# Kernel tuning notes

Measured on AMD Instinct MI355X. Metric: run time of the kernel, lower is better.

Reference implementation:

```python
import jax, jax.numpy as jnp
import numpy as np

N, E, D, R = 50000, 600000, 128, 8


def rgcn_conv(x, src, dst, etype, W, root, bias):
    """PyG-style RGCNConv with mean aggregation per relation.
    x: [N, Din]; W: [R, Din, Dout]; root: [Din, Dout]; bias: [Dout]."""
    n = x.shape[0]
    r = W.shape[0]
    # Transform once per relation at node level (cheaper than per-edge matmul).
    xw = jnp.einsum('nd,rdo->rno', x, W)  # [R, N, Dout]
    # Per-(relation, target) edge counts for mean normalization.
    seg = etype * n + dst                  # combined segment id in [0, R*N)
    counts = jax.ops.segment_sum(jnp.ones(src.shape, dtype=x.dtype), seg,
                                 num_segments=r * n)
    norm = 1.0 / jnp.maximum(counts[seg], 1.0)   # [E]
    msg = xw[etype, src] * norm[:, None]          # gather per edge, [E, Dout]
    agg = jax.ops.segment_sum(msg, dst, num_segments=n)  # scatter-add, [N, Dout]
    return agg + x @ root + bias


def setup_inputs() -> dict:
    key = jax.random.key(0)
    ks = jax.random.split(key, 16)
    s = 1.0 / np.sqrt(D)
    inp = {
        'x': jax.random.normal(ks[0], (N, D), dtype=jnp.float32),
        'edge_index': jax.random.randint(ks[1], (2, E), 0, N, dtype=jnp.int32),
        'edge_type': jax.random.randint(ks[2], (E,), 0, R, dtype=jnp.int32),
        'W1': jax.random.normal(ks[3], (R, D, D), dtype=jnp.float32) * s,
        'root1': jax.random.normal(ks[4], (D, D), dtype=jnp.float32) * s,
        'b1': jnp.zeros((D,), dtype=jnp.float32),
        'W2': jax.random.normal(ks[5], (R, D, D), dtype=jnp.float32) * s,
        'root2': jax.random.normal(ks[6], (D, D), dtype=jnp.float32) * s,
        'b2': jnp.zeros((D,), dtype=jnp.float32),
        'W3': jax.random.normal(ks[7], (R, D, D), dtype=jnp.float32) * s,
        'root3': jax.random.normal(ks[8], (D, D), dtype=jnp.float32) * s,
        'b3': jnp.zeros((D,), dtype=jnp.float32),
        'res_w': jax.random.normal(ks[9], (D, D), dtype=jnp.float32) * s,
        'res_b': jnp.zeros((D,), dtype=jnp.float32),
    }
    return inp


def reference(x, edge_index, edge_type, W1, root1, b1, W2, root2, b2,
              W3, root3, b3, res_w, res_b):
    src, dst = edge_index[0], edge_index[1]
    res = x @ res_w + res_b
    h = jax.nn.relu(rgcn_conv(x, src, dst, edge_type, W1, root1, b1))
    h = res + jax.nn.relu(h)
    h = jax.nn.relu(rgcn_conv(h, src, dst, edge_type, W2, root2, b2))
    h = res + jax.nn.relu(h)
    h = jax.nn.relu(rgcn_conv(h, src, dst, edge_type, W3, root3, b3))
    h = res + jax.nn.relu(h)
    # Dropout(0.05) is identity in eval mode.
    return h
```

## Files before the change

kernel.cpp:

```cpp
#include <hip/hip_runtime.h>
#include <hip/hip_bf16.h>

#define NN 50000
#define EE 600000
#define RR 8
#define NSEG (NN*RR)
#define NB_SCAN ((NSEG + 1023)/1024)

typedef unsigned int u32;
typedef __attribute__((ext_vector_type(8))) short bf16x8;
typedef __attribute__((ext_vector_type(4))) float f32x4;
typedef __attribute__((ext_vector_type(4))) u32 u32x4;

__device__ inline unsigned short f2bf(float f){
  u32 u = __float_as_uint(f);
  u32 r = (u + 0x7fffu + ((u >> 16) & 1u)) >> 16;
  return (unsigned short)r;
}
__device__ inline float bf2f(unsigned short b){ return __uint_as_float((u32)b << 16); }

#define GLD16(g, l)  __builtin_amdgcn_global_load_lds( \
    (const __attribute__((address_space(1))) void*)(g), \
    (__attribute__((address_space(3))) void*)(l), 16, 0, 0)

__global__ void cvt_k(const float* __restrict__ in, unsigned short* __restrict__ out, int n4){
  int i = blockIdx.x * 256 + threadIdx.x;
  if (i >= n4) return;
  float4 v = ((const float4*)in)[i];
  ushort4 o;
  o.x = f2bf(v.x); o.y = f2bf(v.y); o.z = f2bf(v.z); o.w = f2bf(v.w);
  ((ushort4*)out)[i] = o;
}

__global__ void pack_k(const float* __restrict__ Wrel, const float* __restrict__ root,
                       short* __restrict__ Bp, int nk32, int krel){
  int tid = blockIdx.x * 256 + threadIdx.x;
  if (tid >= nk32 * 512) return;
  int lane = tid & 63;
  int nf   = (tid >> 6) & 7;
  int k32  = tid >> 9;
  int col  = nf * 16 + (lane & 15);
  short vals[8];
#pragma unroll
  for (int i = 0; i < 8; ++i){
    int kk = k32 * 32 + ((lane >> 4) << 3) + i;
    float f = (kk < krel) ? Wrel[(size_t)kk * 128 + col]
                          : root[(size_t)(kk - krel) * 128 + col];
    vals[i] = (short)f2bf(f);
  }
  *(bf16x8*)(Bp + (size_t)tid * 8) = *(const bf16x8*)vals;
}

__global__ void count_k(const int* __restrict__ dst, const int* __restrict__ et,
                        u32* __restrict__ cnt){
  int e = blockIdx.x * 256 + threadIdx.x;
  if (e >= EE) return;
  atomicAdd(&cnt[(size_t)et[e] * NN + dst[e]], 1u);
}

__global__ void scan1_k(const u32* __restrict__ cnt, u32* __restrict__ offs, u32* __restrict__ bsum){
  __shared__ u32 s[512];
  int t = threadIdx.x;
  int base = blockIdx.x * 1024 + t * 4;
  u32 loc[4]; u32 sum = 0;
#pragma unroll
  for (int i = 0; i < 4; ++i){ loc[i] = (base + i < NSEG) ? cnt[base + i] : 0u; sum += loc[i]; }
  int pb = 0;
  s[t] = sum; __syncthreads();
  for (int off = 1; off < 256; off <<= 1){
    u32 v = s[pb * 256 + t];
    if (t >= off) v += s[pb * 256 + t - off];
    s[(pb ^ 1) * 256 + t] = v; pb ^= 1; __syncthreads();
  }
  u32 incl = s[pb * 256 + t];
  u32 excl = incl - sum;
  if (t == 255) bsum[blockIdx.x] = incl;
  u32 run = excl;
#pragma unroll
  for (int i = 0; i < 4; ++i){ if (base + i < NSEG) offs[base + i] = run; run += loc[i]; }
}

__global__ void scan2_k(u32* __restrict__ bsum){
  __shared__ u32 s[1024];
  int t = threadIdx.x;
  u32 v = (t < NB_SCAN) ? bsum[t] : 0u;
  int pb = 0;
  s[t] = v; __syncthreads();
  for (int off = 1; off < 512; off <<= 1){
    u32 x = s[pb * 512 + t];
    if (t >= off) x += s[pb * 512 + t - off];
    s[(pb ^ 1) * 512 + t] = x; pb ^= 1; __syncthreads();
  }
  u32 incl = s[pb * 512 + t];
  if (t < NB_SCAN) bsum[t] = incl - v;
}

__global__ void scan3_k(u32* __restrict__ offs, const u32* __restrict__ bsum){
  int t = threadIdx.x;
  int base = blockIdx.x * 1024 + t * 4;
  u32 add = bsum[blockIdx.x];
#pragma unroll
  for (int i = 0; i < 4; ++i){ if (base + i < NSEG) offs[base + i] += add; }
  if (blockIdx.x == 0 && t == 0) offs[NSEG] = EE;
}

__global__ void fill_k(const int* __restrict__ src, const int* __restrict__ dst,
                       const int* __restrict__ et, const u32* __restrict__ offs,
                       u32* __restrict__ cnt, int* __restrict__ elist){
  int e = blockIdx.x * 256 + threadIdx.x;
  if (e >= EE) return;
  int s = et[e] * NN + dst[e];
  u32 p = atomicSub(&cnt[s], 1u);
  elist[offs[s] + p - 1] = src[e];
}

__launch_bounds__(256, 8)
__global__ void agg_k(const u32* __restrict__ offs, const int* __restrict__ elist,
                      const unsigned short* __restrict__ h, unsigned short* __restrict__ a){
  int t = threadIdx.x;
  int g = t >> 3, ll8 = t & 7;
  int seg = blockIdx.x * 32 + g;
  u32 beg = offs[seg], end = offs[seg + 1];
  float s[16];
#pragma unroll
  for (int i = 0; i < 16; ++i) s[i] = 0.f;
  const unsigned short* hb = h + (size_t)ll8 * 16;
  u32 e = beg;
  for (; e + 2 <= end; e += 2){
    int s0 = elist[e], s1 = elist[e + 1];
    const unsigned short* r0 = hb + (size_t)s0 * 128;
    const unsigned short* r1 = hb + (size_t)s1 * 128;
    u32x4 p00 = *(const u32x4*)r0, p01 = *(const u32x4*)(r0 + 8);
    u32x4 p10 = *(const u32x4*)r1, p11 = *(const u32x4*)(r1 + 8);
#pragma unroll
    for (int i = 0; i < 4; ++i){
      s[2*i]     += __uint_as_float(p00[i] << 16)         + __uint_as_float(p10[i] << 16);
      s[2*i+1]   += __uint_as_float(p00[i] & 0xffff0000u) + __uint_as_float(p10[i] & 0xffff0000u);
      s[8+2*i]   += __uint_as_float(p01[i] << 16)         + __uint_as_float(p11[i] << 16);
      s[8+2*i+1] += __uint_as_float(p01[i] & 0xffff0000u) + __uint_as_float(p11[i] & 0xffff0000u);
    }
  }
  if (e < end){
    int s0 = elist[e];
    const unsigned short* r0 = hb + (size_t)s0 * 128;
    u32x4 p00 = *(const u32x4*)r0, p01 = *(const u32x4*)(r0 + 8);
#pragma unroll
    for (int i = 0; i < 4; ++i){
      s[2*i]     += __uint_as_float(p00[i] << 16);
      s[2*i+1]   += __uint_as_float(p00[i] & 0xffff0000u);
      s[8+2*i]   += __uint_as_float(p01[i] << 16);
      s[8+2*i+1] += __uint_as_float(p01[i] & 0xffff0000u);
    }
  }
  u32 deg = end - beg;
  if (deg){
    float inv = 1.f / (float)deg;
#pragma unroll
    for (int i = 0; i < 16; ++i) s[i] *= inv;
  }
  u32x4 o0, o1;
#pragma unroll
  for (int i = 0; i < 4; ++i){
    o0[i] = (u32)f2bf(s[2*i])   | ((u32)f2bf(s[2*i+1])   << 16);
    o1[i] = (u32)f2bf(s[8+2*i]) | ((u32)f2bf(s[8+2*i+1]) << 16);
  }
  unsigned short* ap = a + (size_t)seg * 128 + ll8 * 16;
  *(u32x4*)ap = o0;
  *(u32x4*)(ap + 8) = o1;
}

__launch_bounds__(256, 4)
__global__ void resg_k(const unsigned short* __restrict__ xb, const short* __restrict__ Bp,
                       const float* __restrict__ rb, unsigned short* __restrict__ resb){
  const int tid = threadIdx.x;
  const int w = tid >> 6, l = tid & 63;
  const int sub = l >> 4, llr = l & 15;
  const int rowbase = blockIdx.x * 64 + w * 16;
  int vr = rowbase + llr; if (vr > NN - 1) vr = NN - 1;
  f32x4 acc[8] = {};
#pragma unroll
  for (int t = 0; t < 4; ++t){
    bf16x8 af = *(const bf16x8*)(xb + (size_t)vr * 128 + (t * 4 + sub) * 8);
    const short* bb = Bp + (size_t)(t * 8) * 512 + l * 8;
#pragma unroll
    for (int nf = 0; nf < 8; ++nf){
      bf16x8 bq = *(const bf16x8*)(bb + nf * 512);
      acc[nf] = __builtin_amdgcn_mfma_f32_16x16x32_bf16(af, bq, acc[nf], 0, 0, 0);
    }
  }
  const int lr = l >> 4, lc = l & 15;
#pragma unroll
  for (int nf = 0; nf < 8; ++nf){
    int col = nf * 16 + lc;
    float bv = rb[col];
#pragma unroll
    for (int r = 0; r < 4; ++r){
      int row = rowbase + lr * 4 + r;
      if (row < NN) resb[(size_t)row * 128 + col] = f2bf(acc[nf][r] + bv);
    }
  }
}

template<int OUTMODE>
__launch_bounds__(256, 3)
__global__ void gemm_k(const unsigned short* __restrict__ Aa,
                       const unsigned short* __restrict__ Ah,
                       const short* __restrict__ Bp,
                       const float* __restrict__ bias,
                       const unsigned short* __restrict__ resb,
                       float* __restrict__ outf, unsigned short* __restrict__ outb){
  __shared__ short lds[12288];
  const int tid = threadIdx.x;
  const int w = tid >> 6, l = tid & 63;
  const int wm = w >> 1, wn = w & 1;
  const int sub = l >> 4, llr = l & 15;
  const int mbase = blockIdx.x * 64;
  const size_t plane = (size_t)NN * 128;
  f32x4 acc[2][4] = {};

  int arow = mbase + l; if (arow > NN - 1) arow = NN - 1;

#pragma unroll 1
  for (int kt = 0; kt < 18; ++kt){
    const unsigned short* abase = (kt < 16)
        ? Aa + (size_t)(kt >> 1) * plane + (size_t)(kt & 1) * 64
        : Ah + (size_t)(kt - 16) * 64;
    GLD16(abase + (size_t)arow * 128 + w * 8,       lds + (size_t)(w * 64) * 8);
    GLD16(abase + (size_t)arow * 128 + (4 + w) * 8, lds + (size_t)(256 + w * 64) * 8);
    const short* bsrc = Bp + (size_t)kt * 8192;
#pragma unroll
    for (int i = 0; i < 4; ++i)
      GLD16(bsrc + (size_t)(i * 256 + tid) * 8, lds + (size_t)(4096 + (i * 256 + w * 64) * 8));
    __syncthreads();
#pragma unroll
    for (int t = 0; t < 2; ++t){
      bf16x8 af0 = *(const bf16x8*)(lds + (size_t)(((t * 4 + sub) * 64) + wm * 32 + llr) * 8);
      bf16x8 af1 = *(const bf16x8*)(lds + (size_t)(((t * 4 + sub) * 64) + wm * 32 + 16 + llr) * 8);
#pragma unroll
      for (int nf = 0; nf < 4; ++nf){
        bf16x8 bq = *(const bf16x8*)(lds + (size_t)(4096 + (t * 8 + wn * 4 + nf) * 512 + l * 8));
        acc[0][nf] = __builtin_amdgcn_mfma_f32_16x16x32_bf16(af0, bq, acc[0][nf], 0, 0, 0);
        acc[1][nf] = __builtin_amdgcn_mfma_f32_16x16x32_bf16(af1, bq, acc[1][nf], 0, 0, 0);
      }
    }
    __syncthreads();
  }

  const int lr = l >> 4, lc = l & 15;
#pragma unroll
  for (int mf = 0; mf < 2; ++mf){
#pragma unroll
    for (int nf = 0; nf < 4; ++nf){
      int col = wn * 64 + nf * 16 + lc;
      float bv = bias[col];
#pragma unroll
      for (int r = 0; r < 4; ++r){
        int row = mbase + wm * 32 + mf * 16 + lr * 4 + r;
        if (row < NN){
          float v = acc[mf][nf][r] + bv;
          v = bf2f(resb[(size_t)row * 128 + col]) + fmaxf(v, 0.f);
          if (OUTMODE == 1) outb[(size_t)row * 128 + col] = f2bf(v);
          else              outf[(size_t)row * 128 + col] = v;
        }
      }
    }
  }
}

extern "C" void kernel_launch(void* const* d_in, const int* in_sizes, int n_in,
                              void* d_out, int out_size, void* d_ws, size_t ws_size,
                              hipStream_t stream){
  const float* x  = (const float*)d_in[0];
  const int*   ei = (const int*)d_in[1];
  const int*   et = (const int*)d_in[2];
  const float* W1 = (const float*)d_in[3];
  const float* r1 = (const float*)d_in[4];
  const float* b1 = (const float*)d_in[5];
  const float* W2 = (const float*)d_in[6];
  const float* r2 = (const float*)d_in[7];
  const float* b2 = (const float*)d_in[8];
  const float* W3 = (const float*)d_in[9];
  const float* r3 = (const float*)d_in[10];
  const float* b3 = (const float*)d_in[11];
  const float* rw = (const float*)d_in[12];
  const float* rb = (const float*)d_in[13];
  const int* srcv = ei;
  const int* dstv = ei + EE;

  char* p = (char*)d_ws;
  auto take = [&](size_t b)->char*{ char* q = p; p += (b + 255) & ~(size_t)255; return q; };
  unsigned short* a    = (unsigned short*)take((size_t)NN * 1024 * 2);
  unsigned short* xb   = (unsigned short*)take((size_t)NN * 128 * 2);
  unsigned short* h1   = (unsigned short*)take((size_t)NN * 128 * 2);
  unsigned short* h2   = (unsigned short*)take((size_t)NN * 128 * 2);
  unsigned short* resb = (unsigned short*)take((size_t)NN * 128 * 2);
  short* Bp1 = (short*)take(36 * 4096 * 2);
  short* Bp2 = (short*)take(36 * 4096 * 2);
  short* Bp3 = (short*)take(36 * 4096 * 2);
  short* BpR = (short*)take(4 * 4096 * 2);
  u32* cnt   = (u32*)take((size_t)NSEG * 4);
  u32* offs  = (u32*)take((size_t)(NSEG + 1) * 4);
  int* elist = (int*)take((size_t)EE * 4);
  u32* bsum  = (u32*)take((size_t)NB_SCAN * 4);

  hipMemsetAsync(cnt, 0, (size_t)NSEG * 4, stream);

  cvt_k<<<(NN * 128 / 4 + 255) / 256, 256, 0, stream>>>(x, xb, NN * 128 / 4);
  pack_k<<<(36 * 512 + 255) / 256, 256, 0, stream>>>(W1, r1, Bp1, 36, 1024);
  pack_k<<<(36 * 512 + 255) / 256, 256, 0, stream>>>(W2, r2, Bp2, 36, 1024);
  pack_k<<<(36 * 512 + 255) / 256, 256, 0, stream>>>(W3, r3, Bp3, 36, 1024);
  pack_k<<<(4 * 512 + 255) / 256, 256, 0, stream>>>(nullptr, rw, BpR, 4, 0);

  count_k<<<(EE + 255) / 256, 256, 0, stream>>>(dstv, et, cnt);
  scan1_k<<<NB_SCAN, 256, 0, stream>>>(cnt, offs, bsum);
  scan2_k<<<1, 512, 0, stream>>>(bsum);
  scan3_k<<<NB_SCAN, 256, 0, stream>>>(offs, bsum);
  fill_k<<<(EE + 255) / 256, 256, 0, stream>>>(srcv, dstv, et, offs, cnt, elist);

  const int GB = (NN + 63) / 64;

  resg_k<<<GB, 256, 0, stream>>>(xb, BpR, rb, resb);

  agg_k<<<NSEG / 32, 256, 0, stream>>>(offs, elist, xb, a);
  gemm_k<1><<<GB, 256, 0, stream>>>(a, xb, Bp1, b1, resb, nullptr, h1);
  agg_k<<<NSEG / 32, 256, 0, stream>>>(offs, elist, h1, a);
  gemm_k<1><<<GB, 256, 0, stream>>>(a, h1, Bp2, b2, resb, nullptr, h2);
  agg_k<<<NSEG / 32, 256, 0, stream>>>(offs, elist, h2, a);
  gemm_k<2><<<GB, 256, 0, stream>>>(a, h2, Bp3, b3, resb, (float*)d_out, nullptr);
}
```

Before: 347.4 us.

## Halve GEMM row tile and unroll aggregation gather loop by four

```diff
diff --git a/kernel.cpp b/kernel.cpp
--- a/kernel.cpp
+++ b/kernel.cpp
@@ -114,7 +114,16 @@
   elist[offs[s] + p - 1] = src[e];
 }
 
-__launch_bounds__(256, 8)
+#define ACC1(P0, P1) do{ \
+  _Pragma("unroll") \
+  for (int i_ = 0; i_ < 4; ++i_){ \
+    s[2*i_]     += __uint_as_float((P0)[i_] << 16); \
+    s[2*i_+1]   += __uint_as_float((P0)[i_] & 0xffff0000u); \
+    s[8+2*i_]   += __uint_as_float((P1)[i_] << 16); \
+    s[8+2*i_+1] += __uint_as_float((P1)[i_] & 0xffff0000u); \
+  } }while(0)
+
+__launch_bounds__(256, 6)
 __global__ void agg_k(const u32* __restrict__ offs, const int* __restrict__ elist,
                       const unsigned short* __restrict__ h, unsigned short* __restrict__ a){
   int t = threadIdx.x;
@@ -126,31 +135,32 @@
   for (int i = 0; i < 16; ++i) s[i] = 0.f;
   const unsigned short* hb = h + (size_t)ll8 * 16;
   u32 e = beg;
-  for (; e + 2 <= end; e += 2){
-    int s0 = elist[e], s1 = elist[e + 1];
+  for (; e + 4 <= end; e += 4){
+    int s0 = elist[e], s1 = elist[e+1], s2 = elist[e+2], s3 = elist[e+3];
+    const unsigned short* r0 = hb + (size_t)s0 * 128;
+    const unsigned short* r1 = hb + (size_t)s1 * 128;
+    const unsigned short* r2 = hb + (size_t)s2 * 128;
+    const unsigned short* r3 = hb + (size_t)s3 * 128;
+    u32x4 p00 = *(const u32x4*)r0, p01 = *(const u32x4*)(r0 + 8);
+    u32x4 p10 = *(const u32x4*)r1, p11 = *(const u32x4*)(r1 + 8);
+    u32x4 p20 = *(const u32x4*)r2, p21 = *(const u32x4*)(r2 + 8);
+    u32x4 p30 = *(const u32x4*)r3, p31 = *(const u32x4*)(r3 + 8);
+    ACC1(p00, p01); ACC1(p10, p11); ACC1(p20, p21); ACC1(p30, p31);
+  }
+  if (e + 2 <= end){
+    int s0 = elist[e], s1 = elist[e+1];
     const unsigned short* r0 = hb + (size_t)s0 * 128;
     const unsigned short* r1 = hb + (size_t)s1 * 128;
     u32x4 p00 = *(const u32x4*)r0, p01 = *(const u32x4*)(r0 + 8);
     u32x4 p10 = *(const u32x4*)r1, p11 = *(const u32x4*)(r1 + 8);
-#pragma unroll
-    for (int i = 0; i < 4; ++i){
-      s[2*i]     += __uint_as_float(p00[i] << 16)         + __uint_as_float(p10[i] << 16);
-      s[2*i+1]   += __uint_as_float(p00[i] & 0xffff0000u) + __uint_as_float(p10[i] & 0xffff0000u);
-      s[8+2*i]   += __uint_as_float(p01[i] << 16)         + __uint_as_float(p11[i] << 16);
-      s[8+2*i+1] += __uint_as_float(p01[i] & 0xffff0000u) + __uint_as_float(p11[i] & 0xffff0000u);
-    }
+    ACC1(p00, p01); ACC1(p10, p11);
+    e += 2;
   }
   if (e < end){
     int s0 = elist[e];
     const unsigned short* r0 = hb + (size_t)s0 * 128;
     u32x4 p00 = *(const u32x4*)r0, p01 = *(const u32x4*)(r0 + 8);
-#pragma unroll
-    for (int i = 0; i < 4; ++i){
-      s[2*i]     += __uint_as_float(p00[i] << 16);
-      s[2*i+1]   += __uint_as_float(p00[i] & 0xffff0000u);
-      s[8+2*i]   += __uint_as_float(p01[i] << 16);
-      s[8+2*i+1] += __uint_as_float(p01[i] & 0xffff0000u);
-    }
+    ACC1(p00, p01);
   }
   u32 deg = end - beg;
   if (deg){
@@ -202,45 +212,43 @@
 }
 
 template<int OUTMODE>
-__launch_bounds__(256, 3)
+__launch_bounds__(256, 6)
 __global__ void gemm_k(const unsigned short* __restrict__ Aa,
                        const unsigned short* __restrict__ Ah,
                        const short* __restrict__ Bp,
                        const float* __restrict__ bias,
                        const unsigned short* __restrict__ resb,
                        float* __restrict__ outf, unsigned short* __restrict__ outb){
-  __shared__ short lds[12288];
+  __shared__ short lds[10240];
   const int tid = threadIdx.x;
   const int w = tid >> 6, l = tid & 63;
   const int wm = w >> 1, wn = w & 1;
   const int sub = l >> 4, llr = l & 15;
-  const int mbase = blockIdx.x * 64;
+  const int mbase = blockIdx.x * 32;
   const size_t plane = (size_t)NN * 128;
-  f32x4 acc[2][4] = {};
-
-  int arow = mbase + l; if (arow > NN - 1) arow = NN - 1;
+  f32x4 acc[4] = {};
+
+  int arow = mbase + (l & 31); if (arow > NN - 1) arow = NN - 1;
+  const int aq = w * 2 + (l >> 5);
 
 #pragma unroll 1
   for (int kt = 0; kt < 18; ++kt){
     const unsigned short* abase = (kt < 16)
         ? Aa + (size_t)(kt >> 1) * plane + (size_t)(kt & 1) * 64
         : Ah + (size_t)(kt - 16) * 64;
-    GLD16(abase + (size_t)arow * 128 + w * 8,       lds + (size_t)(w * 64) * 8);
-    GLD16(abase + (size_t)arow * 128 + (4 + w) * 8, lds + (size_t)(256 + w * 64) * 8);
+    GLD16(abase + (size_t)arow * 128 + aq * 8, lds + (size_t)(w * 64) * 8);
     const short* bsrc = Bp + (size_t)kt * 8192;
 #pragma unroll
     for (int i = 0; i < 4; ++i)
-      GLD16(bsrc + (size_t)(i * 256 + tid) * 8, lds + (size_t)(4096 + (i * 256 + w * 64) * 8));
+      GLD16(bsrc + (size_t)(i * 256 + tid) * 8, lds + (size_t)(2048 + (i * 256 + w * 64) * 8));
     __syncthreads();
 #pragma unroll
     for (int t = 0; t < 2; ++t){
-      bf16x8 af0 = *(const bf16x8*)(lds + (size_t)(((t * 4 + sub) * 64) + wm * 32 + llr) * 8);
-      bf16x8 af1 = *(const bf16x8*)(lds + (size_t)(((t * 4 + sub) * 64) + wm * 32 + 16 + llr) * 8);
+      bf16x8 af = *(const bf16x8*)(lds + (size_t)((t * 4 + sub) * 32 + wm * 16 + llr) * 8);
 #pragma unroll
       for (int nf = 0; nf < 4; ++nf){
-        bf16x8 bq = *(const bf16x8*)(lds + (size_t)(4096 + (t * 8 + wn * 4 + nf) * 512 + l * 8));
-        acc[0][nf] = __builtin_amdgcn_mfma_f32_16x16x32_bf16(af0, bq, acc[0][nf], 0, 0, 0);
-        acc[1][nf] = __builtin_amdgcn_mfma_f32_16x16x32_bf16(af1, bq, acc[1][nf], 0, 0, 0);
+        bf16x8 bq = *(const bf16x8*)(lds + (size_t)(2048 + (t * 8 + wn * 4 + nf) * 512 + l * 8));
+        acc[nf] = __builtin_amdgcn_mfma_f32_16x16x32_bf16(af, bq, acc[nf], 0, 0, 0);
       }
     }
     __syncthreads();
@@ -248,20 +256,17 @@
 
   const int lr = l >> 4, lc = l & 15;
 #pragma unroll
-  for (int mf = 0; mf < 2; ++mf){
-#pragma unroll
-    for (int nf = 0; nf < 4; ++nf){
-      int col = wn * 64 + nf * 16 + lc;
-      float bv = bias[col];
-#pragma unroll
-      for (int r = 0; r < 4; ++r){
-        int row = mbase + wm * 32 + mf * 16 + lr * 4 + r;
-        if (row < NN){
-          float v = acc[mf][nf][r] + bv;
-          v = bf2f(resb[(size_t)row * 128 + col]) + fmaxf(v, 0.f);
-          if (OUTMODE == 1) outb[(size_t)row * 128 + col] = f2bf(v);
-          else              outf[(size_t)row * 128 + col] = v;
-        }
+  for (int nf = 0; nf < 4; ++nf){
+    int col = wn * 64 + nf * 16 + lc;
+    float bv = bias[col];
+#pragma unroll
+    for (int r = 0; r < 4; ++r){
+      int row = mbase + wm * 16 + lr * 4 + r;
+      if (row < NN){
+        float v = acc[nf][r] + bv;
+        v = bf2f(resb[(size_t)row * 128 + col]) + fmaxf(v, 0.f);
+        if (OUTMODE == 1) outb[(size_t)row * 128 + col] = f2bf(v);
+        else              outf[(size_t)row * 128 + col] = v;
       }
     }
   }
@@ -317,9 +322,9 @@
   scan3_k<<<NB_SCAN, 256, 0, stream>>>(offs, bsum);
   fill_k<<<(EE + 255) / 256, 256, 0, stream>>>(srcv, dstv, et, offs, cnt, elist);
 
-  const int GB = (NN + 63) / 64;
-
-  resg_k<<<GB, 256, 0, stream>>>(xb, BpR, rb, resb);
+  const int GB = (NN + 31) / 32;
+
+  resg_k<<<(NN + 63) / 64, 256, 0, stream>>>(xb, BpR, rb, resb);
 
   agg_k<<<NSEG / 32, 256, 0, stream>>>(offs, elist, xb, a);
   gemm_k<1><<<GB, 256, 0, stream>>>(a, xb, Bp1, b1, resb, nullptr, h1);
```

Result: faster. 339.9 us (-2.2%).
